# Kernel tuning notes

Hardware: AMD Instinct MI355X
Metric: run time of the kernel (lower is better)

## Reference

```python
import jax, jax.numpy as jnp
import numpy as np

D_MODEL = 2048
N_HEADS = 16
HEAD_DIM = D_MODEL // N_HEADS  # 128
B, T = 2, 1024
XL_LEN = 1024


def setup_inputs() -> dict:
    key = jax.random.key(0)
    ks = jax.random.split(key, 8)
    # rotary angles for head_dim/2 pairs (llama-style)
    inv_freq = 1.0 / (10000.0 ** (jnp.arange(0, HEAD_DIM, 2, dtype=jnp.float32) / HEAD_DIM))
    t = jnp.arange(T, dtype=jnp.float32)
    freqs = jnp.outer(t, inv_freq)  # [T, HEAD_DIM//2]
    return {
        "x": jax.random.normal(ks[0], (B, T, D_MODEL), dtype=jnp.float32),
        "cos": jnp.cos(freqs),
        "sin": jnp.sin(freqs),
        "k_xl": jax.random.normal(ks[1], (B, XL_LEN, D_MODEL), dtype=jnp.float32),
        "v_xl": jax.random.normal(ks[2], (B, XL_LEN, D_MODEL), dtype=jnp.float32),
        "pos_emb": jax.random.normal(ks[3], (XL_LEN, D_MODEL), dtype=jnp.float32) * 0.02,
        "w_qkv": jax.random.normal(ks[4], (3 * D_MODEL, D_MODEL), dtype=jnp.float32) * 0.02,
        "w_proj": jax.random.normal(ks[5], (D_MODEL, D_MODEL), dtype=jnp.float32) * 0.02,
        "is_causal": 0,
    }


def _apply_rope(x, cos, sin):
    # x: [B, T, H, hd]; cos/sin: [T, hd//2]
    xr = x.reshape(*x.shape[:-1], HEAD_DIM // 2, 2)
    x1, x2 = xr[..., 0], xr[..., 1]
    c = cos[None, :, None, :]
    s = sin[None, :, None, :]
    o1 = x1 * c - x2 * s
    o2 = x1 * s + x2 * c
    return jnp.stack([o1, o2], axis=-1).reshape(x.shape)


def reference(x, cos, sin, k_xl, v_xl, pos_emb, w_qkv, w_proj, is_causal):
    Bq, Tq, C = x.shape
    H, hd = N_HEADS, HEAD_DIM
    qkv = jnp.einsum('btc,fc->btf', x, w_qkv)  # fused QKV projection
    q, k, v = jnp.split(qkv, 3, axis=-1)
    # add learned XL positional embedding to cached keys (self.k_xl += emb(arange))
    k_xl = k_xl + pos_emb[None, :, :]
    q = q.reshape(Bq, Tq, H, hd)
    k = k.reshape(Bq, -1, H, hd)
    v = v.reshape(Bq, -1, H, hd)
    q = _apply_rope(q, cos, sin)
    k = _apply_rope(k, cos, sin)
    q = q.transpose(0, 2, 1, 3)  # [B,H,T,hd]
    k = k.transpose(0, 2, 1, 3)
    v = v.transpose(0, 2, 1, 3)
    k_xl_h = k_xl.reshape(Bq, -1, H, hd).transpose(0, 2, 1, 3)
    v_xl_h = v_xl.reshape(Bq, -1, H, hd).transpose(0, 2, 1, 3)
    k_full = jnp.concatenate([k_xl_h, k], axis=-2)  # [B,H,XL+T,hd]
    v_full = jnp.concatenate([v_xl_h, v], axis=-2)
    scale = 1.0 / jnp.sqrt(jnp.asarray(hd, dtype=q.dtype))
    scores = jnp.einsum('bhqd,bhkd->bhqk', q, k_full) * scale
    if is_causal:
        Kv = k_full.shape[-2]
        qi = jnp.arange(Tq)[:, None]
        ki = jnp.arange(Kv)[None, :]
        scores = jnp.where(ki <= qi + (Kv - Tq), scores, jnp.finfo(scores.dtype).min)
    attn = jax.nn.softmax(scores, axis=-1)
    y = jnp.einsum('bhqk,bhkd->bhqd', attn, v_full)
    y = y.transpose(0, 2, 1, 3).reshape(Bq, Tq, C)
    return jnp.einsum('btc,oc->bto', y, w_proj)
```

## Files before the change

### kernel.cpp

```cpp
#include <hip/hip_runtime.h>
#include <stdint.h>

typedef unsigned short u16;
typedef __attribute__((ext_vector_type(4))) float f32x4;
typedef __attribute__((ext_vector_type(8))) short bf16x8;
typedef __attribute__((ext_vector_type(4))) uint32_t u32x4;

#define D_MODEL 2048
#define NHEADS 16
#define HD 128
#define BSZ 2
#define TQ 1024
#define XL 1024
#define KVLEN 2048

__device__ __forceinline__ float b2f(u16 u) {
  union { uint32_t i; float f; } x; x.i = ((uint32_t)u) << 16; return x.f;
}
__device__ __forceinline__ u16 f2b(float f) {
  union { float f; uint32_t i; } x; x.f = f;
  uint32_t r = x.i + 0x7FFFu + ((x.i >> 16) & 1u);
  return (u16)(r >> 16);
}

union U4 { u32x4 u; u16 s[8]; };

__device__ __forceinline__ void async_copy16(const u16* g, u16* l) {
  __builtin_amdgcn_global_load_lds((__attribute__((address_space(1))) void*)g,
                                   (__attribute__((address_space(3))) void*)l,
                                   16, 0, 0);
}

__device__ __forceinline__ float rmax16(float v) {
  v = fmaxf(v, __shfl_xor(v, 1));
  v = fmaxf(v, __shfl_xor(v, 2));
  v = fmaxf(v, __shfl_xor(v, 4));
  v = fmaxf(v, __shfl_xor(v, 8));
  return v;
}
__device__ __forceinline__ float rsum16(float v) {
  v += __shfl_xor(v, 1);
  v += __shfl_xor(v, 2);
  v += __shfl_xor(v, 4);
  v += __shfl_xor(v, 8);
  return v;
}

struct PrefF32 {
  f32x4 lo, hi;
  __device__ __forceinline__ void load(const float* base, size_t off) {
    lo = *(const f32x4*)(base + off);
    hi = *(const f32x4*)(base + off + 4);
  }
  __device__ __forceinline__ u32x4 pack() const {
    U4 o;
    o.s[0] = f2b(lo[0]); o.s[1] = f2b(lo[1]); o.s[2] = f2b(lo[2]); o.s[3] = f2b(lo[3]);
    o.s[4] = f2b(hi[0]); o.s[5] = f2b(hi[1]); o.s[6] = f2b(hi[2]); o.s[7] = f2b(hi[3]);
    return o.u;
  }
};

__global__ __launch_bounds__(256, 4) void cvt_bf16(
    const float* __restrict__ src, u16* __restrict__ dst)
{
  const size_t id = (size_t)blockIdx.x * 256 + threadIdx.x;
  PrefF32 p; p.load(src, id * 8);
  *(u32x4*)&dst[id * 8] = p.pack();
}

template <int BN, bool CSPLIT>
__global__ __launch_bounds__(256, 2) void gemm_bt(
    const u16* __restrict__ A, const u16* __restrict__ B,
    void* __restrict__ C0, void* __restrict__ C1, void* __restrict__ C2,
    int M, int N, int K)
{
  constexpr int JN = BN / 32;
  __shared__ u16 sA[128 * 32];
  __shared__ u16 sB[BN * 32];
  const int tid  = threadIdx.x;
  const int lane = tid & 63;
  const int wave = tid >> 6;
  const int quad = lane >> 4;
  const int mcol = lane & 15;
  const int wm = (wave >> 1) * 64;
  const int wn = (wave & 1) * (BN / 2);
  const int bm = blockIdx.y * 128;
  const int bnE = blockIdx.x * BN;

  f32x4 acc[4][JN] = {};

  const int c0 = tid, c1 = tid + 256;
  size_t a0 = (size_t)(bm + (c0 >> 2)) * K + (c0 & 3) * 8;
  size_t a1 = (size_t)(bm + (c1 >> 2)) * K + (c1 & 3) * 8;
  size_t b0 = (size_t)(bnE + (c0 >> 2)) * K + (c0 & 3) * 8;
  size_t b1 = (BN == 128) ? (size_t)(bnE + (c1 >> 2)) * K + (c1 & 3) * 8 : 0;

  const int nk = K >> 5;
  for (int kk = 0; kk < nk; ++kk) {
    async_copy16(A + a0, &sA[c0 * 8]);
    async_copy16(A + a1, &sA[c1 * 8]);
    async_copy16(B + b0, &sB[c0 * 8]);
    if (BN == 128) async_copy16(B + b1, &sB[c1 * 8]);
    a0 += 32; a1 += 32; b0 += 32; b1 += 32;
    __syncthreads();
    bf16x8 af[4], bff[JN];
#pragma unroll
    for (int i = 0; i < 4; ++i)
      af[i] = *(const bf16x8*)&sA[(wm + i * 16 + mcol) * 32 + quad * 8];
#pragma unroll
    for (int j = 0; j < JN; ++j)
      bff[j] = *(const bf16x8*)&sB[(wn + j * 16 + mcol) * 32 + quad * 8];
#pragma unroll
    for (int i = 0; i < 4; ++i)
#pragma unroll
      for (int j = 0; j < JN; ++j)
        acc[i][j] = __builtin_amdgcn_mfma_f32_16x16x32_bf16(af[i], bff[j], acc[i][j], 0, 0, 0);
    __syncthreads();
  }

  if (CSPLIT) {
    const int sel = bnE >> 11;
    u16* Cp = (u16*)(sel == 0 ? C0 : (sel == 1 ? C1 : C2));
    const int bnl = (bnE & 2047) + wn;
#pragma unroll
    for (int i = 0; i < 4; ++i)
#pragma unroll
      for (int r = 0; r < 4; ++r) {
        const size_t base = (size_t)(bm + wm + i * 16 + quad * 4 + r) * 2048 + bnl;
#pragma unroll
        for (int j = 0; j < JN; ++j)
          Cp[base + j * 16 + mcol] = f2b(acc[i][j][r]);
      }
  } else {
    float* Cp = (float*)C0;
#pragma unroll
    for (int i = 0; i < 4; ++i)
#pragma unroll
      for (int r = 0; r < 4; ++r) {
        const size_t base = (size_t)(bm + wm + i * 16 + quad * 4 + r) * N + bnE + wn;
#pragma unroll
        for (int j = 0; j < JN; ++j)
          Cp[base + j * 16 + mcol] = acc[i][j][r];
      }
  }
}

__global__ __launch_bounds__(256, 4) void prep_k(
    const float* __restrict__ kxl, const float* __restrict__ pos,
    const u16* __restrict__ kbuf, const float* __restrict__ cosw,
    const float* __restrict__ sinw, u16* __restrict__ kfull)
{
  const int id = blockIdx.x * 256 + threadIdx.x;
  const int dc = id & 15;
  const int kv = (id >> 4) & 2047;
  const int bh = id >> 15;
  const int b = bh >> 4, h = bh & 15;
  const int d0 = dc * 8;
  U4 o;
  if (kv < XL) {
    const float* kp = kxl + ((size_t)b * XL + kv) * D_MODEL + h * HD + d0;
    const float* pp = pos + (size_t)kv * D_MODEL + h * HD + d0;
    f32x4 kl = *(const f32x4*)kp, kh = *(const f32x4*)(kp + 4);
    f32x4 pl = *(const f32x4*)pp, ph = *(const f32x4*)(pp + 4);
#pragma unroll
    for (int p = 0; p < 4; ++p) {
      o.s[p]     = f2b(kl[p] + pl[p]);
      o.s[4 + p] = f2b(kh[p] + ph[p]);
    }
  } else {
    const int tq = kv - XL;
    U4 kv_;
    kv_.u = *(const u32x4*)(kbuf + ((size_t)b * TQ + tq) * D_MODEL + h * HD + d0);
    f32x4 cv = *(const f32x4*)(cosw + tq * 64 + (d0 >> 1));
    f32x4 sv = *(const f32x4*)(sinw + tq * 64 + (d0 >> 1));
#pragma unroll
    for (int p = 0; p < 4; ++p) {
      const float e = b2f(kv_.s[2 * p]), od = b2f(kv_.s[2 * p + 1]);
      o.s[2 * p]     = f2b(e * cv[p] - od * sv[p]);
      o.s[2 * p + 1] = f2b(e * sv[p] + od * cv[p]);
    }
  }
  *(u32x4*)&kfull[((size_t)bh * KVLEN + kv) * HD + d0] = o.u;
}

__global__ __launch_bounds__(256, 4) void transpose_v(
    const float* __restrict__ v_xl, const u16* __restrict__ vbuf, u16* __restrict__ vt)
{
  __shared__ u16 tile[64 * 72];
  const int tid = threadIdx.x;
  const int kv0 = blockIdx.x * 64;
  const int d0  = blockIdx.y * 64;
  const int bh  = blockIdx.z;
  const int b = bh >> 4, h = bh & 15;
#pragma unroll
  for (int j = 0; j < 2; ++j) {
    const int id = tid + 256 * j;
    const int kr = id >> 3, dq = (id & 7) * 8;
    const int kvg = kv0 + kr;
    if (kvg < XL) {
      const float* src = v_xl + ((size_t)b * XL + kvg) * D_MODEL + h * HD + d0 + dq;
      PrefF32 p; p.load(src, 0);
      *(u32x4*)&tile[kr * 72 + dq] = p.pack();
    } else {
      const u16* src = vbuf + ((size_t)b * TQ + (kvg - XL)) * D_MODEL + h * HD + d0 + dq;
      *(u32x4*)&tile[kr * 72 + dq] = *(const u32x4*)src;
    }
  }
  __syncthreads();
#pragma unroll
  for (int j = 0; j < 2; ++j) {
    const int id = tid + 256 * j;
    const int dr = id >> 3, kq = (id & 7) * 8;
    U4 ov;
#pragma unroll
    for (int i = 0; i < 8; ++i) ov.s[i] = tile[(kq + i) * 72 + dr];
    *(u32x4*)&vt[((size_t)bh * HD + d0 + dr) * KVLEN + kv0 + kq] = ov.u;
  }
}

#define LSTR 136

__global__ __launch_bounds__(256, 2) void attn(
    const u16* __restrict__ q, const u16* __restrict__ kfull,
    const u16* __restrict__ vt, const float* __restrict__ cosw,
    const float* __restrict__ sinw, const int* __restrict__ iscausal,
    u16* __restrict__ y)
{
  __shared__ u16 sK[128 * LSTR];
  __shared__ u16 sV[128 * LSTR];

  const int tid  = threadIdx.x;
  const int lane = tid & 63;
  const int w    = tid >> 6;
  const int quad = lane >> 4;
  const int mcol = lane & 15;
  const int lin = blockIdx.x + 16 * blockIdx.y;
  const int qt  = (lin >> 3) & 15;
  const int bh  = (lin & 7) + 8 * (lin >> 7);
  const int b = bh >> 4, h = bh & 15;
  const int causal = *iscausal;
  const float SC = 0.08838834764831845f;

  bf16x8 qf[4];
  {
    const int trow = qt * 64 + w * 16 + mcol;
    const u16* qrow = q + ((size_t)b * TQ + trow) * D_MODEL + h * HD;
    const float* crow = cosw + trow * 64;
    const float* srow = sinw + trow * 64;
#pragma unroll
    for (int ks = 0; ks < 4; ++ks) {
      const int d0 = ks * 32 + quad * 8;
      U4 qv; qv.u = *(const u32x4*)(qrow + d0);
      f32x4 cv = *(const f32x4*)(crow + (d0 >> 1));
      f32x4 sv = *(const f32x4*)(srow + (d0 >> 1));
      bf16x8 dst;
#pragma unroll
      for (int p = 0; p < 4; ++p) {
        const float e = b2f(qv.s[2 * p]), o = b2f(qv.s[2 * p + 1]);
        const float re = fmaf(-o, sv[p], e * cv[p]);
        const float im = fmaf( o, cv[p], e * sv[p]);
        dst[2 * p]     = (short)f2b(re * SC);
        dst[2 * p + 1] = (short)f2b(im * SC);
      }
      qf[ks] = dst;
    }
  }

  const int srow = tid >> 4;
  const int sc8 = (tid & 15) * 8;
  const u16* kbase = kfull + (size_t)bh * KVLEN * HD;
  const u16* vbase = vt + (size_t)bh * HD * KVLEN;

  u32x4 kreg[8], vreg[8];
#define LOADT(KV0)                                                          \
  do {                                                                      \
    _Pragma("unroll") for (int j = 0; j < 8; ++j) {                         \
      const int rr = srow + 16 * j;                                         \
      kreg[j] = *(const u32x4*)(kbase + ((size_t)(KV0) + rr) * HD + sc8);   \
      vreg[j] = *(const u32x4*)(vbase + (size_t)rr * KVLEN + (KV0) + sc8);  \
    }                                                                       \
  } while (0)

  f32x4 oacc[8] = {};
  float mrun[4], lrun[4];
#pragma unroll
  for (int r = 0; r < 4; ++r) { mrun[r] = -3.0e38f; lrun[r] = 0.f; }

  LOADT(0);
  for (int t16 = 0; t16 < 16; ++t16) {
    __syncthreads();
#pragma unroll
    for (int j = 0; j < 8; ++j) {
      const int rr = srow + 16 * j;
      *(u32x4*)&sK[rr * LSTR + sc8] = kreg[j];
      *(u32x4*)&sV[rr * LSTR + sc8] = vreg[j];
    }
    __syncthreads();
    if (t16 < 15) LOADT((t16 + 1) * 128);

    const int kv0 = t16 * 128;

    f32x4 s[8] = {};
#pragma unroll
    for (int ks = 0; ks < 4; ++ks) {
      const int cc = ks * 4 + quad;
#pragma unroll
      for (int nt = 0; nt < 8; ++nt) {
        bf16x8 kf = *(const bf16x8*)&sK[(nt * 16 + mcol) * LSTR + cc * 8];
        s[nt] = __builtin_amdgcn_mfma_f32_16x16x32_bf16(qf[ks], kf, s[nt], 0, 0, 0);
      }
    }
    if (causal) {
#pragma unroll
      for (int r = 0; r < 4; ++r) {
        const int qi = qt * 64 + w * 16 + quad * 4 + r;
#pragma unroll
        for (int nt = 0; nt < 8; ++nt) {
          const int ki = kv0 + nt * 16 + mcol;
          if (ki > qi + (KVLEN - TQ)) s[nt][r] = -1.0e30f;
        }
      }
    }

#pragma unroll
    for (int r = 0; r < 4; ++r) {
      float tm = -3.0e38f;
#pragma unroll
      for (int nt = 0; nt < 8; ++nt) tm = fmaxf(tm, s[nt][r]);
      tm = rmax16(tm);
      const float mo = mrun[r];
      const float mn = fmaxf(mo, tm);
      mrun[r] = mn;
      const float al = __expf(mo - mn);
      float rs = 0.f;
#pragma unroll
      for (int nt = 0; nt < 8; ++nt) {
        const float p = __expf(s[nt][r] - mn);
        s[nt][r] = p;
        rs += p;
      }
      rs = rsum16(rs);
      lrun[r] = lrun[r] * al + rs;
#pragma unroll
      for (int nd = 0; nd < 8; ++nd) oacc[nd][r] *= al;
    }
    __syncthreads();

    u16* sPw = &sK[w * 16 * LSTR];
#pragma unroll
    for (int r = 0; r < 4; ++r) {
      const int row = quad * 4 + r;
#pragma unroll
      for (int nt = 0; nt < 8; ++nt)
        sPw[row * LSTR + nt * 16 + mcol] = f2b(s[nt][r]);
    }

#pragma unroll
    for (int ks = 0; ks < 4; ++ks) {
      const int cc = ks * 4 + quad;
      bf16x8 pa = *(const bf16x8*)&sPw[mcol * LSTR + cc * 8];
#pragma unroll
      for (int nd = 0; nd < 8; ++nd) {
        bf16x8 vf = *(const bf16x8*)&sV[(nd * 16 + mcol) * LSTR + cc * 8];
        oacc[nd] = __builtin_amdgcn_mfma_f32_16x16x32_bf16(pa, vf, oacc[nd], 0, 0, 0);
      }
    }
  }
#undef LOADT

#pragma unroll
  for (int r = 0; r < 4; ++r) {
    const int trow = qt * 64 + w * 16 + quad * 4 + r;
    const float inv = 1.0f / lrun[r];
    u16* yr = y + ((size_t)b * TQ + trow) * D_MODEL + h * HD;
#pragma unroll
    for (int nd = 0; nd < 8; ++nd)
      yr[nd * 16 + mcol] = f2b(oacc[nd][r] * inv);
  }
}

extern "C" void kernel_launch(void* const* d_in, const int* in_sizes, int n_in,
                              void* d_out, int out_size, void* d_ws, size_t ws_size,
                              hipStream_t stream) {
  const float* x      = (const float*)d_in[0];
  const float* cosw   = (const float*)d_in[1];
  const float* sinw   = (const float*)d_in[2];
  const float* k_xl   = (const float*)d_in[3];
  const float* v_xl   = (const float*)d_in[4];
  const float* pos    = (const float*)d_in[5];
  const float* w_qkv  = (const float*)d_in[6];
  const float* w_proj = (const float*)d_in[7];
  const int* isc      = (const int*)d_in[8];
  float* out = (float*)d_out;

  char* ws = (char*)d_ws;
  u16* qbuf  = (u16*)ws;
  u16* kbuf  = (u16*)(ws + (size_t)8388608);
  u16* vbuf  = (u16*)(ws + (size_t)16777216);
  u16* wqb   = (u16*)(ws + (size_t)25165824);
  u16* kfull = (u16*)(ws + (size_t)25165824);
  u16* wpb   = (u16*)(ws + (size_t)25165824);
  u16* vt    = (u16*)(ws + (size_t)41943040);
  u16* xb    = (u16*)(ws + (size_t)50331648);
  u16* y_ws  = kbuf;

  cvt_bf16<<<2048, 256, 0, stream>>>(x, xb);
  cvt_bf16<<<6144, 256, 0, stream>>>(w_qkv, wqb);

  dim3 g1(48, 16);
  gemm_bt<128, true><<<g1, 256, 0, stream>>>(xb, wqb, qbuf, kbuf, vbuf, 2048, 6144, 2048);

  prep_k<<<4096, 256, 0, stream>>>(k_xl, pos, kbuf, cosw, sinw, kfull);

  dim3 gt(KVLEN / 64, HD / 64, BSZ * NHEADS);
  transpose_v<<<gt, 256, 0, stream>>>(v_xl, vbuf, vt);

  dim3 ga(16, BSZ * NHEADS);
  attn<<<ga, 256, 0, stream>>>(qbuf, kfull, vt, cosw, sinw, isc, y_ws);

  cvt_bf16<<<2048, 256, 0, stream>>>(w_proj, wpb);

  dim3 g2(32, 16);
  gemm_bt<64, false><<<g2, 256, 0, stream>>>(y_ws, wpb, out, nullptr, nullptr, 2048, 2048, 2048);
}
```

Measured before the change: 346.7 us.

## Compute transposed scores so softmax probabilities feed PV MFMA from registers

```diff
diff --git a/kernel.cpp b/kernel.cpp
--- a/kernel.cpp
+++ b/kernel.cpp
@@ -29,21 +29,6 @@
   __builtin_amdgcn_global_load_lds((__attribute__((address_space(1))) void*)g,
                                    (__attribute__((address_space(3))) void*)l,
                                    16, 0, 0);
-}
-
-__device__ __forceinline__ float rmax16(float v) {
-  v = fmaxf(v, __shfl_xor(v, 1));
-  v = fmaxf(v, __shfl_xor(v, 2));
-  v = fmaxf(v, __shfl_xor(v, 4));
-  v = fmaxf(v, __shfl_xor(v, 8));
-  return v;
-}
-__device__ __forceinline__ float rsum16(float v) {
-  v += __shfl_xor(v, 1);
-  v += __shfl_xor(v, 2);
-  v += __shfl_xor(v, 4);
-  v += __shfl_xor(v, 8);
-  return v;
 }
 
 struct PrefF32 {
@@ -282,9 +267,8 @@
   } while (0)
 
   f32x4 oacc[8] = {};
-  float mrun[4], lrun[4];
-#pragma unroll
-  for (int r = 0; r < 4; ++r) { mrun[r] = -3.0e38f; lrun[r] = 0.f; }
+  float mrun = -3.0e38f;
+  float lrun = 0.f;
 
   LOADT(0);
   for (int t16 = 0; t16 < 16; ++t16) {
@@ -307,71 +291,85 @@
 #pragma unroll
       for (int nt = 0; nt < 8; ++nt) {
         bf16x8 kf = *(const bf16x8*)&sK[(nt * 16 + mcol) * LSTR + cc * 8];
-        s[nt] = __builtin_amdgcn_mfma_f32_16x16x32_bf16(qf[ks], kf, s[nt], 0, 0, 0);
+        s[nt] = __builtin_amdgcn_mfma_f32_16x16x32_bf16(kf, qf[ks], s[nt], 0, 0, 0);
       }
     }
     if (causal) {
-#pragma unroll
-      for (int r = 0; r < 4; ++r) {
-        const int qi = qt * 64 + w * 16 + quad * 4 + r;
-#pragma unroll
-        for (int nt = 0; nt < 8; ++nt) {
-          const int ki = kv0 + nt * 16 + mcol;
+      const int qi = qt * 64 + w * 16 + mcol;
+#pragma unroll
+      for (int nt = 0; nt < 8; ++nt)
+#pragma unroll
+        for (int r = 0; r < 4; ++r) {
+          const int ki = kv0 + nt * 16 + quad * 4 + r;
           if (ki > qi + (KVLEN - TQ)) s[nt][r] = -1.0e30f;
         }
-      }
-    }
-
-#pragma unroll
-    for (int r = 0; r < 4; ++r) {
-      float tm = -3.0e38f;
-#pragma unroll
-      for (int nt = 0; nt < 8; ++nt) tm = fmaxf(tm, s[nt][r]);
-      tm = rmax16(tm);
-      const float mo = mrun[r];
-      const float mn = fmaxf(mo, tm);
-      mrun[r] = mn;
-      const float al = __expf(mo - mn);
-      float rs = 0.f;
-#pragma unroll
-      for (int nt = 0; nt < 8; ++nt) {
+    }
+
+    float tm = -3.0e38f;
+#pragma unroll
+    for (int nt = 0; nt < 8; ++nt) {
+      const float t01 = fmaxf(s[nt][0], s[nt][1]);
+      const float t23 = fmaxf(s[nt][2], s[nt][3]);
+      tm = fmaxf(tm, fmaxf(t01, t23));
+    }
+    tm = fmaxf(tm, __shfl_xor(tm, 16));
+    tm = fmaxf(tm, __shfl_xor(tm, 32));
+    const float mo = mrun;
+    const float mn = fmaxf(mo, tm);
+    mrun = mn;
+    const float al = __expf(mo - mn);
+    float rs = 0.f;
+#pragma unroll
+    for (int nt = 0; nt < 8; ++nt)
+#pragma unroll
+      for (int r = 0; r < 4; ++r) {
         const float p = __expf(s[nt][r] - mn);
         s[nt][r] = p;
         rs += p;
       }
-      rs = rsum16(rs);
-      lrun[r] = lrun[r] * al + rs;
-#pragma unroll
-      for (int nd = 0; nd < 8; ++nd) oacc[nd][r] *= al;
-    }
-    __syncthreads();
-
-    u16* sPw = &sK[w * 16 * LSTR];
-#pragma unroll
-    for (int r = 0; r < 4; ++r) {
-      const int row = quad * 4 + r;
-#pragma unroll
-      for (int nt = 0; nt < 8; ++nt)
-        sPw[row * LSTR + nt * 16 + mcol] = f2b(s[nt][r]);
-    }
+    rs += __shfl_xor(rs, 16);
+    rs += __shfl_xor(rs, 32);
+    lrun = lrun * al + rs;
+
+    float al4[4];
+#pragma unroll
+    for (int r = 0; r < 4; ++r)
+      al4[r] = __shfl(al, (lane & 48) + quad * 4 + r);
+#pragma unroll
+    for (int nd = 0; nd < 8; ++nd)
+#pragma unroll
+      for (int r = 0; r < 4; ++r) oacc[nd][r] *= al4[r];
 
 #pragma unroll
     for (int ks = 0; ks < 4; ++ks) {
-      const int cc = ks * 4 + quad;
-      bf16x8 pa = *(const bf16x8*)&sPw[mcol * LSTR + cc * 8];
+      U4 pa;
+#pragma unroll
+      for (int e = 0; e < 4; ++e) {
+        pa.s[e]     = f2b(s[2 * ks][e]);
+        pa.s[4 + e] = f2b(s[2 * ks + 1][e]);
+      }
+      const int kvlo = 32 * ks + 4 * quad;
 #pragma unroll
       for (int nd = 0; nd < 8; ++nd) {
-        bf16x8 vf = *(const bf16x8*)&sV[(nd * 16 + mcol) * LSTR + cc * 8];
-        oacc[nd] = __builtin_amdgcn_mfma_f32_16x16x32_bf16(pa, vf, oacc[nd], 0, 0, 0);
+        const u16* vrow = &sV[(nd * 16 + mcol) * LSTR + kvlo];
+        U4 vf;
+        *(uint2*)&vf.s[0] = *(const uint2*)(vrow);
+        *(uint2*)&vf.s[4] = *(const uint2*)(vrow + 16);
+        oacc[nd] = __builtin_amdgcn_mfma_f32_16x16x32_bf16(
+            *(const bf16x8*)&pa, *(const bf16x8*)&vf, oacc[nd], 0, 0, 0);
       }
     }
   }
 #undef LOADT
 
+  float lq[4];
+#pragma unroll
+  for (int r = 0; r < 4; ++r)
+    lq[r] = __shfl(lrun, (lane & 48) + quad * 4 + r);
 #pragma unroll
   for (int r = 0; r < 4; ++r) {
     const int trow = qt * 64 + w * 16 + quad * 4 + r;
-    const float inv = 1.0f / lrun[r];
+    const float inv = 1.0f / lq[r];
     u16* yr = y + ((size_t)b * TQ + trow) * D_MODEL + h * HD;
 #pragma unroll
     for (int nd = 0; nd < 8; ++nd)
```

New measurement: 343.4 us. About the same (-0.9%).
